# Kernel optimization log

Hardware: AMD Instinct MI355X
Metric: run time of the kernel (lower is better)

The kernel has to match this reference:

```python
import jax, jax.numpy as jnp
import numpy as np

B, H, L, D = 4, 8, 2048, 64
FACTOR = 5
U = FACTOR * int(np.ceil(np.log(L)))  # sample_k == n_top == 40


def setup_inputs() -> dict:
    key = jax.random.key(0)
    kq, kk, kv, ki = jax.random.split(key, 4)
    return {
        "queries": jax.random.normal(kq, (B, L, H, D), dtype=jnp.float32),
        "keys": jax.random.normal(kk, (B, L, H, D), dtype=jnp.float32),
        "values": jax.random.normal(kv, (B, L, H, D), dtype=jnp.float32),
        "attn_mask": jnp.zeros((1,), dtype=bool),
        "random_index": jax.random.randint(ki, (L, U), 0, L),
    }


def _prob_attention(queries, keys, values, random_index):
    Bq, L_Q, Hq, Dq = queries.shape
    L_K = keys.shape[1]
    q = jnp.transpose(queries, (0, 2, 1, 3))  # [B,H,L_Q,D]
    k = jnp.transpose(keys, (0, 2, 1, 3))     # [B,H,L_K,D]
    v = jnp.transpose(values, (0, 2, 1, 3))   # [B,H,L_V,D]
    n_top = min(FACTOR * int(np.ceil(np.log(L_Q))), L_Q)

    # --- ProbSparse query scoring: sample K per query, M = max - mean ---
    k_samp = k[:, :, random_index, :]                        # [B,H,L_Q,S,D] gather
    qk_samp = jnp.einsum('bhqd,bhqsd->bhqs', q, k_samp)      # [B,H,L_Q,S]
    M = qk_samp.max(axis=-1) - qk_samp.sum(axis=-1) / L_K    # [B,H,L_Q]
    _, top_idx = jax.lax.top_k(M, n_top)                     # [B,H,n_top]

    # --- dense scores only for the top queries ---
    q_sel = jnp.take_along_axis(q, top_idx[..., None], axis=2)  # [B,H,n_top,D]
    scale = 1.0 / jnp.sqrt(jnp.asarray(Dq, jnp.float32))        # self.scale or 1/sqrt(D)
    scores = jnp.einsum('bhud,bhkd->bhuk', q_sel, k) * scale    # [B,H,n_top,L_K]

    # --- ProbMask: causal mask rows gathered at selected query positions ---
    causal = jnp.triu(jnp.ones((L_Q, L_K), dtype=bool), 1)
    scores = jnp.where(causal[top_idx], -jnp.inf, scores)
    attn = jax.nn.softmax(scores, axis=-1)

    # --- initial context = cumsum(V) (mask_flag=True), scatter updates ---
    ctx = jnp.cumsum(v, axis=2)                              # [B,H,L_Q,D]
    upd = jnp.einsum('bhuk,bhkd->bhud', attn, v)             # [B,H,n_top,D]
    b_idx = jnp.arange(Bq)[:, None, None]
    h_idx = jnp.arange(Hq)[None, :, None]
    ctx = ctx.at[b_idx, h_idx, top_idx].set(upd)
    return jnp.transpose(ctx, (0, 2, 1, 3))                  # [B,L_Q,H,D]


def reference(queries, keys, values, attn_mask, random_index):
    # attn_mask is ignored by the torch module (it builds its own ProbMask).
    return _prob_attention(queries, keys, values, random_index)
```

## Files before the change

kernel.cpp:

```cpp
#include <hip/hip_runtime.h>

#define Bd 4
#define Hd 8
#define Ld 2048
#define Dd 64
#define Ud 40
#define NTOP 40
#define NCHUNK 64
#define CSZ 32

#define NS 16
#define FTILE 128
#define QSTR 68
#define KSTR 68
#define PSTR 132

__global__ __launch_bounds__(256) void phase1_kernel(
    const float* __restrict__ q, const float* __restrict__ k,
    const float* __restrict__ v, const int* __restrict__ ridx,
    float* __restrict__ M, float* __restrict__ csum) {
  __shared__ float red[256];
  int tid = threadIdx.x;
  if (blockIdx.x < 2048) {
    const int nblk = 2048;
    int orig = blockIdx.x;
    int bid = (orig & 7) * (nblk >> 3) + (orig >> 3);
    int gw = bid * 4 + (tid >> 6);
    int lane = tid & 63;
    int hg = lane >> 3;
    int s8 = lane & 7;
    int b = gw >> 11;
    int l = gw & (Ld - 1);

    const float* qrow = q + ((size_t)b * Ld + l) * (Hd * Dd) + lane * 8;
    float4 q0 = *reinterpret_cast<const float4*>(qrow);
    float4 q1 = *reinterpret_cast<const float4*>(qrow + 4);

    int rv = 0;
    if (lane < Ud) rv = ridx[l * Ud + lane];
    const float* kb = k + (size_t)b * Ld * (Hd * Dd);

    float mx = -INFINITY, sm = 0.f;
#pragma unroll 8
    for (int u = 0; u < Ud; ++u) {
      int kidx = __shfl(rv, u);
      const float* kr = kb + (size_t)kidx * (Hd * Dd) + lane * 8;
      float4 k0 = *reinterpret_cast<const float4*>(kr);
      float4 k1 = *reinterpret_cast<const float4*>(kr + 4);
      float dot = q0.x * k0.x + q0.y * k0.y + q0.z * k0.z + q0.w * k0.w +
                  q1.x * k1.x + q1.y * k1.y + q1.z * k1.z + q1.w * k1.w;
      dot += __shfl_xor(dot, 1);
      dot += __shfl_xor(dot, 2);
      dot += __shfl_xor(dot, 4);
      mx = fmaxf(mx, dot);
      sm += dot;
    }
    if (s8 == 0)
      M[((size_t)b * Hd + hg) * Ld + l] = mx - sm * (1.0f / (float)Ld);
  } else {
    int n = blockIdx.x - 2048;
    int c = n & (NCHUNK - 1), bh = n >> 6;
    int b = bh >> 3, h = bh & 7;
    int d = tid & 63, jg = tid >> 6;
    int t0 = c * CSZ;
    float s = 0.f;
#pragma unroll
    for (int j = jg; j < CSZ; j += 4)
      s += v[(((size_t)b * Ld + t0 + j) * Hd + h) * Dd + d];
    red[tid] = s;
    __syncthreads();
    if (jg == 0)
      csum[(size_t)n * Dd + d] =
          red[d] + red[64 + d] + red[128 + d] + red[192 + d];
  }
}

__global__ __launch_bounds__(64) void phase2_kernel(const float* __restrict__ M,
                                                    int* __restrict__ topIdx,
                                                    float* __restrict__ csum) {
  int lane = threadIdx.x;
  if (blockIdx.x < 32) {
    int bh = blockIdx.x;
    const float* mrow = M + (size_t)bh * Ld;

    unsigned int key[32];
#pragma unroll
    for (int j = 0; j < 32; ++j) {
      unsigned int bits = __float_as_uint(mrow[lane + j * 64]);
      key[j] = (bits & 0x80000000u) ? ~bits : (bits | 0x80000000u);
    }

    const int ISENT = 1 << 30;
    unsigned int k0 = 0u, k1c = 0u, k2c = 0u;
    int i0 = ISENT, i1c = ISENT, i2c = ISENT;
#pragma unroll
    for (int j = 0; j < 32; ++j) {
      unsigned int kj = key[j];
      int idx = lane + j * 64;
      if (kj > k0) {
        k2c = k1c; i2c = i1c; k1c = k0; i1c = i0; k0 = kj; i0 = idx;
      } else if (kj > k1c) {
        k2c = k1c; i2c = i1c; k1c = kj; i1c = idx;
      } else if (kj > k2c) {
        k2c = kj; i2c = idx;
      }
    }

    for (int it = 0; it < NTOP; ++it) {
      unsigned int wk = k0;
      int wi = i0;
#pragma unroll
      for (int off = 1; off < 64; off <<= 1) {
        unsigned int ok = __shfl_xor(wk, off);
        int oi = __shfl_xor(wi, off);
        if (ok > wk || (ok == wk && oi < wi)) { wk = ok; wi = oi; }
      }
      if (lane == 0) topIdx[bh * NTOP + it] = wi;
      if (wi == i0) {
        k0 = k1c; i0 = i1c; k1c = k2c; i1c = i2c; k2c = 0u; i2c = ISENT;
        if (k0 == 0u) {
          i0 = ISENT; i1c = ISENT; i2c = ISENT;
#pragma unroll
          for (int j = 0; j < 32; ++j) {
            unsigned int kj = key[j];
            int idx = lane + j * 64;
            bool valid = (kj < wk) || (kj == wk && idx > wi);
            kj = valid ? kj : 0u;
            if (kj > k0) {
              k2c = k1c; i2c = i1c; k1c = k0; i1c = i0; k0 = kj; i0 = idx;
            } else if (kj > k1c) {
              k2c = k1c; i2c = i1c; k1c = kj; i1c = idx;
            } else if (kj > k2c) {
              k2c = kj; i2c = idx;
            }
          }
        }
      }
    }
  } else {
    int bh = blockIdx.x - 32;
    float acc = 0.f;
#pragma unroll 8
    for (int c = 0; c < NCHUNK; ++c) {
      size_t i = ((size_t)bh * NCHUNK + c) * Dd + lane;
      float s = csum[i];
      csum[i] = acc;
      acc += s;
    }
  }
}

__global__ __launch_bounds__(256) void phase3_kernel(
    const float* __restrict__ q, const float* __restrict__ k,
    const float* __restrict__ v, const int* __restrict__ topIdx,
    const float* __restrict__ csum, float* __restrict__ out,
    float* __restrict__ Opart, float* __restrict__ mS,
    float* __restrict__ sS) {
  __shared__ float qs[NTOP * QSTR];
  __shared__ float ks[FTILE * KSTR];
  __shared__ float p[NTOP * PSTR];
  __shared__ int ts[NTOP];
  int tid = threadIdx.x;

  if (blockIdx.x >= 512) {
    int m = blockIdx.x - 512;
    int lane = tid & 63, w = tid >> 6;
    int blk = m * 4 + w;
    int c = blk & (NCHUNK - 1), bh = blk >> 6;
    int b = bh >> 3, h = bh & 7;
    float acc = csum[(size_t)blk * Dd + lane];
    int t0 = c * CSZ;
    const float* vp = v + (((size_t)b * Ld + t0) * Hd + h) * Dd + lane;
    float* op = out + (((size_t)b * Ld + t0) * Hd + h) * Dd + lane;
#pragma unroll 8
    for (int j = 0; j < CSZ; ++j) {
      acc += vp[(size_t)j * (Hd * Dd)];
      op[(size_t)j * (Hd * Dd)] = acc;
    }
    return;
  }

  int split = blockIdx.x % NS;
  int bh = blockIdx.x / NS;
  int b = bh >> 3, h = bh & 7;
  int k0 = split * FTILE;

  if (tid < NTOP) ts[tid] = topIdx[bh * NTOP + tid];
  __syncthreads();

  for (int i = tid; i < NTOP * 16; i += 256) {
    int u = i >> 4, ps = i & 15;
    float4 qv = reinterpret_cast<const float4*>(
        q + (((size_t)b * Ld + ts[u]) * Hd + h) * Dd)[ps];
    *reinterpret_cast<float4*>(&qs[u * QSTR + ps * 4]) = qv;
  }
  for (int i = tid; i < FTILE * 16; i += 256) {
    int r = i >> 4, ps = i & 15;
    float4 kv = reinterpret_cast<const float4*>(
        k + (((size_t)b * Ld + k0 + r) * Hd + h) * Dd)[ps];
    *reinterpret_cast<float4*>(&ks[r * KSTR + ps * 4]) = kv;
  }
  __syncthreads();

  int ug = tid & 7, kg = tid >> 3;
  int ub = ug * 5, kb = kg * 4;
  {
    float acc[5][4] = {};
    for (int dd = 0; dd < Dd; dd += 4) {
      float4 kv[4], qv[5];
#pragma unroll
      for (int i = 0; i < 4; ++i)
        kv[i] = *reinterpret_cast<const float4*>(&ks[(kb + i) * KSTR + dd]);
#pragma unroll
      for (int i = 0; i < 5; ++i)
        qv[i] = *reinterpret_cast<const float4*>(&qs[(ub + i) * QSTR + dd]);
#pragma unroll
      for (int ui = 0; ui < 5; ++ui)
#pragma unroll
        for (int ki = 0; ki < 4; ++ki)
          acc[ui][ki] += qv[ui].x * kv[ki].x + qv[ui].y * kv[ki].y +
                         qv[ui].z * kv[ki].z + qv[ui].w * kv[ki].w;
    }
#pragma unroll
    for (int ui = 0; ui < 5; ++ui) {
      int u = ub + ui;
      int t = ts[u];
      float4 o;
      o.x = (k0 + kb + 0 <= t) ? acc[ui][0] * 0.125f : -INFINITY;
      o.y = (k0 + kb + 1 <= t) ? acc[ui][1] * 0.125f : -INFINITY;
      o.z = (k0 + kb + 2 <= t) ? acc[ui][2] * 0.125f : -INFINITY;
      o.w = (k0 + kb + 3 <= t) ? acc[ui][3] * 0.125f : -INFINITY;
      *reinterpret_cast<float4*>(&p[u * PSTR + kb]) = o;
    }
  }
  __syncthreads();

  for (int i = tid; i < FTILE * 16; i += 256) {
    int r = i >> 4, ps = i & 15;
    float4 vv = reinterpret_cast<const float4*>(
        v + (((size_t)b * Ld + k0 + r) * Hd + h) * Dd)[ps];
    *reinterpret_cast<float4*>(&ks[r * KSTR + ps * 4]) = vv;
  }
  if (tid < NTOP * 4) {
    int u = tid >> 2, l4 = tid & 3;
    float* pr = p + u * PSTR;
    float mx = -1e30f;
#pragma unroll 8
    for (int j = l4; j < FTILE; j += 4) mx = fmaxf(mx, pr[j]);
    mx = fmaxf(mx, __shfl_xor(mx, 1));
    mx = fmaxf(mx, __shfl_xor(mx, 2));
    float sum = 0.f;
#pragma unroll 8
    for (int j = l4; j < FTILE; j += 4) {
      float pe = __expf(pr[j] - mx);
      pr[j] = pe;
      sum += pe;
    }
    sum += __shfl_xor(sum, 1);
    sum += __shfl_xor(sum, 2);
    if (l4 == 0) {
      mS[((size_t)bh * NS + split) * NTOP + u] = mx;
      sS[((size_t)bh * NS + split) * NTOP + u] = sum;
    }
  }
  __syncthreads();

  int ug2 = tid >> 5, dg = tid & 31;
  int ub2 = ug2 * 5, d2 = dg * 2;
  float acc[5][2] = {};
#pragma unroll 4
  for (int kk = 0; kk < FTILE; ++kk) {
    float2 vv = *reinterpret_cast<const float2*>(&ks[kk * KSTR + d2]);
#pragma unroll
    for (int i = 0; i < 5; ++i) {
      float pe = p[(ub2 + i) * PSTR + kk];
      acc[i][0] += pe * vv.x;
      acc[i][1] += pe * vv.y;
    }
  }
  float* ob = Opart + ((size_t)bh * NS + split) * (NTOP * Dd);
#pragma unroll
  for (int i = 0; i < 5; ++i)
    *reinterpret_cast<float2*>(&ob[(ub2 + i) * Dd + d2]) =
        make_float2(acc[i][0], acc[i][1]);
}

__global__ __launch_bounds__(64) void flash_combine_kernel(
    const float* __restrict__ Opart, const float* __restrict__ mS,
    const float* __restrict__ sS, const int* __restrict__ topIdx,
    float* __restrict__ out) {
  int row = blockIdx.x;
  int u = row % NTOP, bh = row / NTOP;
  int b = bh >> 3, h = bh & 7;
  int d = threadIdx.x;
  int t = topIdx[row];

  float mg = -1e30f;
#pragma unroll
  for (int s = 0; s < NS; ++s)
    mg = fmaxf(mg, mS[((size_t)bh * NS + s) * NTOP + u]);
  float den = 0.f, o = 0.f;
#pragma unroll
  for (int s = 0; s < NS; ++s) {
    float w = __expf(mS[((size_t)bh * NS + s) * NTOP + u] - mg);
    den += w * sS[((size_t)bh * NS + s) * NTOP + u];
    o += w * Opart[(((size_t)bh * NS + s) * NTOP + u) * Dd + d];
  }
  out[(((size_t)b * Ld + t) * Hd + h) * Dd + d] = o / den;
}

__global__ void cumsum_write_kernel(const float* __restrict__ v,
                                    const float* __restrict__ csum,
                                    float* __restrict__ out) {
  int blk = blockIdx.x;
  int c = blk & (NCHUNK - 1), bh = blk >> 6;
  int b = bh >> 3, h = bh & 7;
  int d = threadIdx.x;
  float acc = csum[(size_t)blk * Dd + d];
  int t0 = c * CSZ;
#pragma unroll 8
  for (int j = 0; j < CSZ; ++j) {
    size_t idx = (((size_t)b * Ld + t0 + j) * Hd + h) * Dd + d;
    acc += v[idx];
    out[idx] = acc;
  }
}

__global__ void attn_update_kernel(const float* __restrict__ q,
                                   const float* __restrict__ k,
                                   const float* __restrict__ v,
                                   const int* __restrict__ topIdx,
                                   float* __restrict__ out) {
  __shared__ float sc[Ld];
  __shared__ float qs[Dd];
  __shared__ float red[256];
  int tid = threadIdx.x;
  int bh = blockIdx.x / NTOP;
  int b = bh >> 3, h = bh & 7;
  int t = topIdx[blockIdx.x];

  if (tid < Dd) qs[tid] = q[(((size_t)b * Ld + t) * Hd + h) * Dd + tid];
  __syncthreads();

  int nk = t + 1;
  const float4* qv4 = reinterpret_cast<const float4*>(qs);
  float lmax = -INFINITY;
  for (int kk = tid; kk < nk; kk += 256) {
    const float4* kr = reinterpret_cast<const float4*>(
        k + (((size_t)b * Ld + kk) * Hd + h) * Dd);
    float dot = 0.f;
#pragma unroll
    for (int j = 0; j < Dd / 4; ++j) {
      float4 a = qv4[j];
      float4 bb = kr[j];
      dot += a.x * bb.x + a.y * bb.y + a.z * bb.z + a.w * bb.w;
    }
    dot *= 0.125f;
    sc[kk] = dot;
    lmax = fmaxf(lmax, dot);
  }
  red[tid] = lmax;
  __syncthreads();
  for (int s = 128; s; s >>= 1) {
    if (tid < s) red[tid] = fmaxf(red[tid], red[tid + s]);
    __syncthreads();
  }
  float m = red[0];
  __syncthreads();
  float lsum = 0.f;
  for (int kk = tid; kk < nk; kk += 256) {
    float pp = __expf(sc[kk] - m);
    sc[kk] = pp;
    lsum += pp;
  }
  red[tid] = lsum;
  __syncthreads();
  for (int s = 128; s; s >>= 1) {
    if (tid < s) red[tid] += red[tid + s];
    __syncthreads();
  }
  float inv_denom = 1.0f / red[0];
  __syncthreads();
  int d = tid & 63, kg = tid >> 6;
  float acc = 0.f;
  for (int kk = kg; kk < nk; kk += 4)
    acc += sc[kk] * v[(((size_t)b * Ld + kk) * Hd + h) * Dd + d];
  red[tid] = acc;
  __syncthreads();
  if (kg == 0) {
    float r = red[d] + red[64 + d] + red[128 + d] + red[192 + d];
    out[(((size_t)b * Ld + t) * Hd + h) * Dd + d] = r * inv_denom;
  }
}

extern "C" void kernel_launch(void* const* d_in, const int* in_sizes, int n_in,
                              void* d_out, int out_size, void* d_ws,
                              size_t ws_size, hipStream_t stream) {
  const float* q = (const float*)d_in[0];
  const float* k = (const float*)d_in[1];
  const float* v = (const float*)d_in[2];
  const int* ridx = (const int*)d_in[4];
  float* out = (float*)d_out;

  char* ws = (char*)d_ws;
  float* M = (float*)(ws + 0);
  int* topIdx = (int*)(ws + 262144);
  float* csum = (float*)(ws + 272384);
  float* Opart = (float*)(ws + 3942400);
  float* mS = (float*)(ws + 9185280);
  float* sS = (float*)(ws + 9267200);
  const size_t need_new = 9349120;

  phase1_kernel<<<4096, 256, 0, stream>>>(q, k, v, ridx, M, csum);
  phase2_kernel<<<64, 64, 0, stream>>>(M, topIdx, csum);

  if (ws_size >= need_new) {
    phase3_kernel<<<1024, 256, 0, stream>>>(q, k, v, topIdx, csum, out, Opart,
                                            mS, sS);
    flash_combine_kernel<<<Bd * Hd * NTOP, 64, 0, stream>>>(Opart, mS, sS,
                                                            topIdx, out);
  } else {
    cumsum_write_kernel<<<Bd * Hd * NCHUNK, 64, 0, stream>>>(v, csum, out);
    attn_update_kernel<<<Bd * Hd * NTOP, 256, 0, stream>>>(q, k, v, topIdx,
                                                           out);
  }
}
```

Measured before the change: 94.77 us.

## Remap phase1 sampling so each lane computes full per-head dot products

The sampled-key scoring in phase1 changes its lane mapping. Each lane now holds one head's full 64-element query row in registers and computes whole dot products for 5 sampled keys. Before, lanes split each dot product 8 ways and reduced with shuffles on every sample. The per-sample shuffle reductions become a single max/sum butterfly at the end, and launch bounds now ask for 4 blocks per CU. The cost is much higher register use for the 16 float4 query values. Each lane's K loads are also less coalesced, since a lane reads 256 contiguous bytes of one row rather than adjacent lanes sharing one row segment.

```diff
diff --git a/kernel.cpp b/kernel.cpp
--- a/kernel.cpp
+++ b/kernel.cpp
@@ -15,7 +15,7 @@
 #define KSTR 68
 #define PSTR 132
 
-__global__ __launch_bounds__(256) void phase1_kernel(
+__global__ __launch_bounds__(256, 4) void phase1_kernel(
     const float* __restrict__ q, const float* __restrict__ k,
     const float* __restrict__ v, const int* __restrict__ ridx,
     float* __restrict__ M, float* __restrict__ csum) {
@@ -27,36 +27,47 @@
     int bid = (orig & 7) * (nblk >> 3) + (orig >> 3);
     int gw = bid * 4 + (tid >> 6);
     int lane = tid & 63;
-    int hg = lane >> 3;
-    int s8 = lane & 7;
+    int s = lane >> 3;
+    int h = lane & 7;
     int b = gw >> 11;
     int l = gw & (Ld - 1);
 
-    const float* qrow = q + ((size_t)b * Ld + l) * (Hd * Dd) + lane * 8;
-    float4 q0 = *reinterpret_cast<const float4*>(qrow);
-    float4 q1 = *reinterpret_cast<const float4*>(qrow + 4);
+    const float4* qr4 = reinterpret_cast<const float4*>(
+        q + ((size_t)b * Ld + l) * (Hd * Dd) + h * Dd);
+    float4 qreg[16];
+#pragma unroll
+    for (int i = 0; i < 16; ++i) qreg[i] = qr4[i];
 
     int rv = 0;
     if (lane < Ud) rv = ridx[l * Ud + lane];
     const float* kb = k + (size_t)b * Ld * (Hd * Dd);
 
     float mx = -INFINITY, sm = 0.f;
-#pragma unroll 8
-    for (int u = 0; u < Ud; ++u) {
-      int kidx = __shfl(rv, u);
-      const float* kr = kb + (size_t)kidx * (Hd * Dd) + lane * 8;
-      float4 k0 = *reinterpret_cast<const float4*>(kr);
-      float4 k1 = *reinterpret_cast<const float4*>(kr + 4);
-      float dot = q0.x * k0.x + q0.y * k0.y + q0.z * k0.z + q0.w * k0.w +
-                  q1.x * k1.x + q1.y * k1.y + q1.z * k1.z + q1.w * k1.w;
-      dot += __shfl_xor(dot, 1);
-      dot += __shfl_xor(dot, 2);
-      dot += __shfl_xor(dot, 4);
-      mx = fmaxf(mx, dot);
-      sm += dot;
-    }
-    if (s8 == 0)
-      M[((size_t)b * Hd + hg) * Ld + l] = mx - sm * (1.0f / (float)Ld);
+#pragma unroll
+    for (int j = 0; j < Ud / 8; ++j) {
+      int row = __shfl(rv, j * 8 + s);
+      const float4* kr4 = reinterpret_cast<const float4*>(
+          kb + (size_t)row * (Hd * Dd) + h * Dd);
+      float4 acc = {0.f, 0.f, 0.f, 0.f};
+#pragma unroll
+      for (int i = 0; i < 16; ++i) {
+        float4 kv = kr4[i];
+        acc.x += qreg[i].x * kv.x;
+        acc.y += qreg[i].y * kv.y;
+        acc.z += qreg[i].z * kv.z;
+        acc.w += qreg[i].w * kv.w;
+      }
+      float d = (acc.x + acc.y) + (acc.z + acc.w);
+      mx = fmaxf(mx, d);
+      sm += d;
+    }
+#pragma unroll
+    for (int off = 8; off < 64; off <<= 1) {
+      mx = fmaxf(mx, __shfl_xor(mx, off));
+      sm += __shfl_xor(sm, off);
+    }
+    if (s == 0)
+      M[((size_t)b * Hd + h) * Ld + l] = mx - sm * (1.0f / (float)Ld);
   } else {
     int n = blockIdx.x - 2048;
     int c = n & (NCHUNK - 1), bh = n >> 6;
```

After: 228.2 us. 2.41x slower.
